# Kernel optimization log

Hardware: AMD Instinct MI355X
Metric: run time of the kernel (lower is better)

Reference implementation:

```python
import jax, jax.numpy as jnp
import numpy as np

TINY = np.finfo(np.float32).tiny


def setup_inputs() -> dict:
    key = jax.random.key(0)
    k1, k2, k3 = jax.random.split(key, 3)
    B, IN, OUT = 4096, 4096, 1024
    x = jax.random.normal(k1, (B, IN), dtype=jnp.float32)
    weight = jax.random.normal(k2, (IN, OUT), dtype=jnp.float32)
    uniform = jax.random.uniform(k3, (IN, OUT), dtype=jnp.float32)
    T = jnp.ones((1,), dtype=jnp.float32)
    return {"x": x, "weight": weight, "uniform": uniform, "T": T}


def reference(x, weight, uniform, T):
    # training-path forward of ConcreteLayer
    # uniform -> (1 - tiny) * u + tiny, then Gumbel noise
    u = (1.0 - TINY) * uniform + TINY
    gumbel = -jnp.log(-jnp.log(u))                      # [in, out]
    noisy_logits = (weight + gumbel) / T                # temperature scaling
    samples = jax.nn.softmax(noisy_logits, axis=1)      # softmax over out dim (torch default for 2D)
    out = jnp.einsum('bi,ik->bk', x, samples)           # [batch, out]
    return out
```

## Files before the change

### kernel.cpp

```cpp
#include <hip/hip_runtime.h>
#include <cstdint>
#include <cstddef>


#define TINYF 1.17549435082228750797e-38f
#define LN2F 0.69314718055994530942f
#define LOG2EF 1.44269504088896340736f

typedef unsigned short u16;
typedef __attribute__((ext_vector_type(8))) short bf16x8;
typedef __attribute__((ext_vector_type(4))) float f32x4;

__device__ __forceinline__ u16 f2bf(float f) {
  union { float f; uint32_t u; } v; v.f = f;
  uint32_t r = v.u + 0x7FFFu + ((v.u >> 16) & 1u);
  return (u16)(r >> 16);
}

__device__ __forceinline__ float log2_hw(float x) { return __builtin_amdgcn_logf(x); }
__device__ __forceinline__ float exp2_hw(float x) { return __builtin_amdgcn_exp2f(x); }

__device__ __forceinline__ float gumbel_fast(float u) {
  float t = -log2_hw(u);
  return -LN2F * log2_hw(t * LN2F);
}
__device__ __forceinline__ float exp_fast(float x) { return exp2_hw(x * LOG2EF); }

__device__ __forceinline__ void gld_lds16(const void* g, void* l) {
  __builtin_amdgcn_global_load_lds(
      (__attribute__((address_space(1))) void*)(g),
      (__attribute__((address_space(3))) void*)(l), 16, 0, 0);
}

__global__ void trans_exp_kernel(const float* __restrict__ W, const float* __restrict__ U,
                                 const float* __restrict__ Tp, u16* __restrict__ BT,
                                 float* __restrict__ d) {
  __shared__ float tile[64][65];
  const int k0 = blockIdx.x * 64, n0 = blockIdx.y * 64;
  const int t = threadIdx.x;
  const float invT = 1.0f / Tp[0];
  {
    const int nn4 = (t & 15) * 4, kq = t >> 4;
#pragma unroll
    for (int r = 0; r < 4; ++r) {
      int kk = r * 16 + kq;
      size_t gi = (size_t)(k0 + kk) * 1024 + (n0 + nn4);
      float4 w = *(const float4*)&W[gi];
      float4 u = *(const float4*)&U[gi];
      float e0 = exp_fast((w.x + gumbel_fast(u.x * (1.0f - TINYF) + TINYF)) * invT);
      float e1 = exp_fast((w.y + gumbel_fast(u.y * (1.0f - TINYF) + TINYF)) * invT);
      float e2 = exp_fast((w.z + gumbel_fast(u.z * (1.0f - TINYF) + TINYF)) * invT);
      float e3 = exp_fast((w.w + gumbel_fast(u.w * (1.0f - TINYF) + TINYF)) * invT);
      tile[kk][nn4 + 0] = e0; tile[kk][nn4 + 1] = e1;
      tile[kk][nn4 + 2] = e2; tile[kk][nn4 + 3] = e3;
      float s = (e0 + e1) + (e2 + e3);
#pragma unroll
      for (int m = 8; m > 0; m >>= 1) s += __shfl_xor(s, m, 16);
      if ((t & 15) == 0) atomicAdd(&d[k0 + kk], s);
    }
  }
  __syncthreads();
  {
    const int kk4 = (t & 15) * 4, nq = t >> 4;
#pragma unroll
    for (int r = 0; r < 4; ++r) {
      int nn = r * 16 + nq;
      ushort4 o;
      o.x = f2bf(tile[kk4 + 0][nn]);
      o.y = f2bf(tile[kk4 + 1][nn]);
      o.z = f2bf(tile[kk4 + 2][nn]);
      o.w = f2bf(tile[kk4 + 3][nn]);
      *(ushort4*)&BT[(size_t)(n0 + nn) * 4096 + (k0 + kk4)] = o;
    }
  }
}

__global__ void cast_zero_kernel(const float4* __restrict__ x, const float4* __restrict__ d4,
                                 ushort4* __restrict__ xb, float4* __restrict__ out,
                                 int n4x, int n4o) {
  int i = blockIdx.x * blockDim.x + threadIdx.x;
  if (i < n4x) {
    int col4 = i & 1023;
    float4 v = x[i];
    float4 dd = d4[col4];
    ushort4 o;
    o.x = f2bf(v.x / dd.x); o.y = f2bf(v.y / dd.y);
    o.z = f2bf(v.z / dd.z); o.w = f2bf(v.w / dd.w);
    xb[i] = o;
  } else {
    int j = i - n4x;
    if (j < n4o) out[j] = make_float4(0.f, 0.f, 0.f, 0.f);
  }
}

#define TM 128
#define TN 128
#define TK 64

__launch_bounds__(256)
__global__ void gemm_bt_kernel(const u16* __restrict__ A, const u16* __restrict__ BT,
                               float* __restrict__ C, int M, int N, int K) {
  __shared__ u16 As[TM * TK];
  __shared__ u16 Bs[TN * TK];

  const int tid = threadIdx.x;
  const int lane = tid & 63, w = tid >> 6;
  const int wm = w >> 1, wn = w & 1;
  const int m0 = blockIdx.x * TM, n0 = blockIdx.y * TN;
  const int quad = lane >> 4, r16 = lane & 15;
  const int srow = lane >> 3;
  const int sg = (lane & 7) ^ srow;

  const int kz = blockIdx.z;
  const int Kh = K >> 1;
  const u16* Ak = A + (size_t)kz * Kh;
  const u16* Bk = BT + (size_t)kz * Kh;

  f32x4 acc[4][4] = {};

  for (int kt = 0; kt < Kh; kt += TK) {
    __syncthreads();
#pragma unroll
    for (int c = 0; c < 4; ++c) {
      int chunk = w * 4 + c;
      gld_lds16(Ak + (size_t)(m0 + chunk * 8 + srow) * K + kt + sg * 8, (char*)As + chunk * 1024);
      gld_lds16(Bk + (size_t)(n0 + chunk * 8 + srow) * K + kt + sg * 8, (char*)Bs + chunk * 1024);
    }
    __syncthreads();

#pragma unroll
    for (int ss = 0; ss < 2; ++ss) {
      bf16x8 aF[4], bF[4];
#pragma unroll
      for (int mi = 0; mi < 4; ++mi) {
        int row = wm * 64 + mi * 16 + r16;
        aF[mi] = *(const bf16x8*)((const char*)As + row * 128 + (((ss * 4 + quad) ^ (row & 7)) * 16));
      }
#pragma unroll
      for (int ni = 0; ni < 4; ++ni) {
        int row = wn * 64 + ni * 16 + r16;
        bF[ni] = *(const bf16x8*)((const char*)Bs + row * 128 + (((ss * 4 + quad) ^ (row & 7)) * 16));
      }
#pragma unroll
      for (int mi = 0; mi < 4; ++mi)
#pragma unroll
        for (int ni = 0; ni < 4; ++ni)
          acc[mi][ni] = __builtin_amdgcn_mfma_f32_16x16x32_bf16(aF[mi], bF[ni], acc[mi][ni], 0, 0, 0);
    }
  }

#pragma unroll
  for (int mi = 0; mi < 4; ++mi)
#pragma unroll
    for (int ni = 0; ni < 4; ++ni)
#pragma unroll
      for (int r = 0; r < 4; ++r) {
        int row = m0 + wm * 64 + mi * 16 + quad * 4 + r;
        int col = n0 + wn * 64 + ni * 16 + r16;
        atomicAdd(&C[(size_t)row * N + col], acc[mi][ni][r]);
      }
}

extern "C" void kernel_launch(void* const* d_in, const int* in_sizes, int n_in,
                              void* d_out, int out_size, void* d_ws, size_t ws_size,
                              hipStream_t stream) {
  const int M = 4096, K = 4096, N = 1024;
  const float* x = (const float*)d_in[0];
  const float* W = (const float*)d_in[1];
  const float* U = (const float*)d_in[2];
  const float* Tp = (const float*)d_in[3];
  float* out = (float*)d_out;

  char* ws = (char*)d_ws;
  u16* xb = (u16*)ws;
  u16* bt = (u16*)(ws + (size_t)M * K * 2);
  float* dsum = (float*)(ws + (size_t)M * K * 2 + (size_t)N * K * 2);

  hipMemsetAsync(dsum, 0, K * sizeof(float), stream);
  trans_exp_kernel<<<dim3(K / 64, N / 64), 256, 0, stream>>>(W, U, Tp, bt, dsum);
  const int n4x = M * K / 4, n4o = M * N / 4;
  cast_zero_kernel<<<dim3((n4x + n4o) / 256), 256, 0, stream>>>(
      (const float4*)x, (const float4*)dsum, (ushort4*)xb, (float4*)out, n4x, n4o);
  gemm_bt_kernel<<<dim3(M / TM, N / TN, 2), 256, 0, stream>>>(xb, bt, out, M, N, K);
}
```

Measured before the change: 196.2 us.

## Fuse prep kernels and move softmax normalization from x onto BT

The memset, exp/transpose kernel and cast/zero kernel are merged into one launch. Row sums are now written as per-block partials rather than accumulated with atomics. The 1/sum normalization moves from the large x cast (16M elements) to a small in-place rescale of BT (4M elements), which lets the x cast run alongside the exp work. In exchange it adds a kernel launch and a second bf16 rounding of BT.

```diff
diff --git a/kernel.cpp b/kernel.cpp
--- a/kernel.cpp
+++ b/kernel.cpp
@@ -16,6 +16,10 @@
   uint32_t r = v.u + 0x7FFFu + ((v.u >> 16) & 1u);
   return (u16)(r >> 16);
 }
+__device__ __forceinline__ float bf2f(u16 h) {
+  union { float f; uint32_t u; } v; v.u = ((uint32_t)h) << 16;
+  return v.f;
+}
 
 __device__ __forceinline__ float log2_hw(float x) { return __builtin_amdgcn_logf(x); }
 __device__ __forceinline__ float exp2_hw(float x) { return __builtin_amdgcn_exp2f(x); }
@@ -32,70 +36,102 @@
       (__attribute__((address_space(3))) void*)(l), 16, 0, 0);
 }
 
-__global__ void trans_exp_kernel(const float* __restrict__ W, const float* __restrict__ U,
-                                 const float* __restrict__ Tp, u16* __restrict__ BT,
-                                 float* __restrict__ d) {
+#define NB_TRANS 1024
+#define NB_CAST 16384
+#define NB_ZERO 4096
+
+__global__ void prep_kernel(const float* __restrict__ W, const float* __restrict__ U,
+                            const float* __restrict__ Tp, const float4* __restrict__ x,
+                            u16* __restrict__ BT, float* __restrict__ dpart,
+                            ushort4* __restrict__ xb, float4* __restrict__ out) {
   __shared__ float tile[64][65];
-  const int k0 = blockIdx.x * 64, n0 = blockIdx.y * 64;
+  const int bx = blockIdx.x;
   const int t = threadIdx.x;
-  const float invT = 1.0f / Tp[0];
-  {
-    const int nn4 = (t & 15) * 4, kq = t >> 4;
-#pragma unroll
-    for (int r = 0; r < 4; ++r) {
-      int kk = r * 16 + kq;
-      size_t gi = (size_t)(k0 + kk) * 1024 + (n0 + nn4);
-      float4 w = *(const float4*)&W[gi];
-      float4 u = *(const float4*)&U[gi];
-      float e0 = exp_fast((w.x + gumbel_fast(u.x * (1.0f - TINYF) + TINYF)) * invT);
-      float e1 = exp_fast((w.y + gumbel_fast(u.y * (1.0f - TINYF) + TINYF)) * invT);
-      float e2 = exp_fast((w.z + gumbel_fast(u.z * (1.0f - TINYF) + TINYF)) * invT);
-      float e3 = exp_fast((w.w + gumbel_fast(u.w * (1.0f - TINYF) + TINYF)) * invT);
-      tile[kk][nn4 + 0] = e0; tile[kk][nn4 + 1] = e1;
-      tile[kk][nn4 + 2] = e2; tile[kk][nn4 + 3] = e3;
-      float s = (e0 + e1) + (e2 + e3);
-#pragma unroll
-      for (int m = 8; m > 0; m >>= 1) s += __shfl_xor(s, m, 16);
-      if ((t & 15) == 0) atomicAdd(&d[k0 + kk], s);
-    }
-  }
-  __syncthreads();
-  {
-    const int kk4 = (t & 15) * 4, nq = t >> 4;
-#pragma unroll
-    for (int r = 0; r < 4; ++r) {
-      int nn = r * 16 + nq;
-      ushort4 o;
-      o.x = f2bf(tile[kk4 + 0][nn]);
-      o.y = f2bf(tile[kk4 + 1][nn]);
-      o.z = f2bf(tile[kk4 + 2][nn]);
-      o.w = f2bf(tile[kk4 + 3][nn]);
-      *(ushort4*)&BT[(size_t)(n0 + nn) * 4096 + (k0 + kk4)] = o;
-    }
-  }
-}
-
-__global__ void cast_zero_kernel(const float4* __restrict__ x, const float4* __restrict__ d4,
-                                 ushort4* __restrict__ xb, float4* __restrict__ out,
-                                 int n4x, int n4o) {
-  int i = blockIdx.x * blockDim.x + threadIdx.x;
-  if (i < n4x) {
-    int col4 = i & 1023;
+
+  if (bx < NB_TRANS) {
+    const int k0 = (bx & 63) * 64, n0 = (bx >> 6) * 64;
+    const float invT = 1.0f / Tp[0];
+    {
+      const int nn4 = (t & 15) * 4, kq = t >> 4;
+#pragma unroll
+      for (int r = 0; r < 4; ++r) {
+        int kk = r * 16 + kq;
+        size_t gi = (size_t)(k0 + kk) * 1024 + (n0 + nn4);
+        float4 w = *(const float4*)&W[gi];
+        float4 u = *(const float4*)&U[gi];
+        float e0 = exp_fast((w.x + gumbel_fast(u.x * (1.0f - TINYF) + TINYF)) * invT);
+        float e1 = exp_fast((w.y + gumbel_fast(u.y * (1.0f - TINYF) + TINYF)) * invT);
+        float e2 = exp_fast((w.z + gumbel_fast(u.z * (1.0f - TINYF) + TINYF)) * invT);
+        float e3 = exp_fast((w.w + gumbel_fast(u.w * (1.0f - TINYF) + TINYF)) * invT);
+        tile[kk][nn4 + 0] = e0; tile[kk][nn4 + 1] = e1;
+        tile[kk][nn4 + 2] = e2; tile[kk][nn4 + 3] = e3;
+        float s = (e0 + e1) + (e2 + e3);
+#pragma unroll
+        for (int m = 8; m > 0; m >>= 1) s += __shfl_xor(s, m, 16);
+        if ((t & 15) == 0) dpart[(bx >> 6) * 4096 + k0 + kk] = s;
+      }
+    }
+    __syncthreads();
+    {
+      const int kk4 = (t & 15) * 4, nq = t >> 4;
+#pragma unroll
+      for (int r = 0; r < 4; ++r) {
+        int nn = r * 16 + nq;
+        ushort4 o;
+        o.x = f2bf(tile[kk4 + 0][nn]);
+        o.y = f2bf(tile[kk4 + 1][nn]);
+        o.z = f2bf(tile[kk4 + 2][nn]);
+        o.w = f2bf(tile[kk4 + 3][nn]);
+        *(ushort4*)&BT[(size_t)(n0 + nn) * 4096 + (k0 + kk4)] = o;
+      }
+    }
+  } else if (bx < NB_TRANS + NB_CAST) {
+    int i = (bx - NB_TRANS) * 256 + t;
     float4 v = x[i];
-    float4 dd = d4[col4];
     ushort4 o;
-    o.x = f2bf(v.x / dd.x); o.y = f2bf(v.y / dd.y);
-    o.z = f2bf(v.z / dd.z); o.w = f2bf(v.w / dd.w);
+    o.x = f2bf(v.x); o.y = f2bf(v.y); o.z = f2bf(v.z); o.w = f2bf(v.w);
     xb[i] = o;
   } else {
-    int j = i - n4x;
-    if (j < n4o) out[j] = make_float4(0.f, 0.f, 0.f, 0.f);
+    int j = (bx - NB_TRANS - NB_CAST) * 256 + t;
+    out[j] = make_float4(0.f, 0.f, 0.f, 0.f);
+  }
+}
+
+__global__ void bt_scale_kernel(u16* __restrict__ BT, const float* __restrict__ dpart) {
+  __shared__ float invd[128];
+  const int c0 = blockIdx.x * 128;
+  const int r0 = blockIdx.y * 128;
+  const int t = threadIdx.x;
+  if (t < 128) {
+    float s = 0.f;
+#pragma unroll
+    for (int p = 0; p < 16; ++p) s += dpart[p * 4096 + c0 + t];
+    invd[t] = 1.0f / s;
+  }
+  __syncthreads();
+  const int cv = (t & 15) * 8, rq = t >> 4;
+  const float4 ia = *(const float4*)&invd[cv];
+  const float4 ib = *(const float4*)&invd[cv + 4];
+#pragma unroll
+  for (int pass = 0; pass < 8; ++pass) {
+    int row = r0 + pass * 16 + rq;
+    size_t gi = (size_t)row * 4096 + c0 + cv;
+    ushort4 a = *(ushort4*)&BT[gi];
+    ushort4 b = *(ushort4*)&BT[gi + 4];
+    ushort4 oa, ob;
+    oa.x = f2bf(bf2f(a.x) * ia.x); oa.y = f2bf(bf2f(a.y) * ia.y);
+    oa.z = f2bf(bf2f(a.z) * ia.z); oa.w = f2bf(bf2f(a.w) * ia.w);
+    ob.x = f2bf(bf2f(b.x) * ib.x); ob.y = f2bf(bf2f(b.y) * ib.y);
+    ob.z = f2bf(bf2f(b.z) * ib.z); ob.w = f2bf(bf2f(b.w) * ib.w);
+    *(ushort4*)&BT[gi] = oa;
+    *(ushort4*)&BT[gi + 4] = ob;
   }
 }
 
 #define TM 128
 #define TN 128
 #define TK 64
+#define SPLITK 2
 
 __launch_bounds__(256)
 __global__ void gemm_bt_kernel(const u16* __restrict__ A, const u16* __restrict__ BT,
@@ -174,12 +210,10 @@
   char* ws = (char*)d_ws;
   u16* xb = (u16*)ws;
   u16* bt = (u16*)(ws + (size_t)M * K * 2);
-  float* dsum = (float*)(ws + (size_t)M * K * 2 + (size_t)N * K * 2);
-
-  hipMemsetAsync(dsum, 0, K * sizeof(float), stream);
-  trans_exp_kernel<<<dim3(K / 64, N / 64), 256, 0, stream>>>(W, U, Tp, bt, dsum);
-  const int n4x = M * K / 4, n4o = M * N / 4;
-  cast_zero_kernel<<<dim3((n4x + n4o) / 256), 256, 0, stream>>>(
-      (const float4*)x, (const float4*)dsum, (ushort4*)xb, (float4*)out, n4x, n4o);
-  gemm_bt_kernel<<<dim3(M / TM, N / TN, 2), 256, 0, stream>>>(xb, bt, out, M, N, K);
-}
+  float* dpart = (float*)(ws + (size_t)M * K * 2 + (size_t)N * K * 2);
+
+  prep_kernel<<<dim3(NB_TRANS + NB_CAST + NB_ZERO), 256, 0, stream>>>(
+      W, U, Tp, (const float4*)x, bt, dpart, (ushort4*)xb, (float4*)out);
+  bt_scale_kernel<<<dim3(32, 8), 256, 0, stream>>>(bt, dpart);
+  gemm_bt_kernel<<<dim3(M / TM, N / TN, SPLITK), 256, 0, stream>>>(xb, bt, out, M, N, K);
+}
```

Result: no change. 192.7 us (-1.8%).
